# Kernel tuning notes

Hardware: AMD Instinct MI355X
Metric: run time of the kernel (lower is better)

## Reference

```python
import jax, jax.numpy as jnp
import numpy as np

WINDOW = 5  # must be odd so conv 'same' output length == tlength


def setup_inputs() -> dict:
    key = jax.random.key(0)
    tlength = 16777216
    return {"factor": jax.random.normal(key, (tlength,), dtype=jnp.float32)}


def reference(factor):
    window = WINDOW
    # moving average: conv1d with ones kernel, padding=window//2 (== 'same' for odd window)
    w = jnp.ones((window,), dtype=factor.dtype)
    moving_average = jnp.convolve(factor, w, mode='same') / window
    # rate of change: 0 followed by squared consecutive differences
    diffs = (moving_average[:-1] - moving_average[1:]) ** 2
    change = jnp.concatenate([jnp.zeros((1,), dtype=factor.dtype), diffs])
    change = change / jnp.sum(change)
    # power-weighted elementwise scaling
    return (1.0 - change) ** 5 * factor
```

## Files before the change

### kernel.cpp

```cpp
#include <hip/hip_runtime.h>


#define BLOCK 256
#define RGRID 2048
#define NBUCKET 16
#define BUCKET_STRIDE 64

typedef __attribute__((ext_vector_type(4))) float vfloat4;

__device__ __forceinline__ float change_term(const float* __restrict__ f, long long i, long long n) {
    if (i < 1) return 0.0f;
    float a = (i >= 3)    ? f[i - 3] : 0.0f;
    float b = (i + 2 < n) ? f[i + 2] : 0.0f;
    float d = a - b;
    return d * d;
}

__device__ __forceinline__ float pow5(float t) {
    float t2 = t * t;
    float t4 = t2 * t2;
    return t4 * t;
}

__device__ __forceinline__ float vec_terms(float4 p, float4 c, float4 q) {
    float d0 = p.y - c.z;
    float d1 = p.z - c.w;
    float d2 = p.w - q.x;
    float d3 = c.x - q.y;
    return d0 * d0 + d1 * d1 + d2 * d2 + d3 * d3;
}

__device__ __forceinline__ vfloat4 vec_out(float4 p, float4 c, float4 q, float inv) {
    float d0 = p.y - c.z;
    float d1 = p.z - c.w;
    float d2 = p.w - q.x;
    float d3 = c.x - q.y;
    vfloat4 o;
    o.x = pow5(1.0f - d0 * d0 * inv) * c.x;
    o.y = pow5(1.0f - d1 * d1 * inv) * c.y;
    o.z = pow5(1.0f - d2 * d2 * inv) * c.z;
    o.w = pow5(1.0f - d3 * d3 * inv) * c.w;
    return o;
}

__global__ __launch_bounds__(BLOCK)
void reduce_change_kernel(const float* __restrict__ f, int nvec, long long n,
                          float* __restrict__ sum_out) {
    const float4* __restrict__ fv = (const float4*)f;
    const int T = RGRID * BLOCK;
    const int tid = blockIdx.x * BLOCK + threadIdx.x;
    const int M = nvec - 2;
    float acc = 0.0f;

    int idx = tid;
    for (; idx + 3 * T < M; idx += 4 * T) {
        float4 p[4], c[4], q[4];
        #pragma unroll
        for (int u = 0; u < 4; ++u) {
            int v = 1 + idx + u * T;
            p[u] = fv[v - 1];
            c[u] = fv[v];
            q[u] = fv[v + 1];
        }
        #pragma unroll
        for (int u = 0; u < 4; ++u)
            acc += vec_terms(p[u], c[u], q[u]);
    }
    for (; idx < M; idx += T) {
        int v = 1 + idx;
        acc += vec_terms(fv[v - 1], fv[v], fv[v + 1]);
    }
    if (tid == 0) {
        #pragma unroll
        for (int k = 0; k < 4; ++k) acc += change_term(f, k, n);
        long long j0 = n - 4;
        #pragma unroll
        for (int k = 0; k < 4; ++k) acc += change_term(f, j0 + k, n);
    }

    #pragma unroll
    for (int off = 32; off > 0; off >>= 1)
        acc += __shfl_down(acc, off, 64);
    __shared__ float smem[4];
    int lane = threadIdx.x & 63;
    int wave = threadIdx.x >> 6;
    if (lane == 0) smem[wave] = acc;
    __syncthreads();
    if (threadIdx.x == 0) {
        float s = smem[0] + smem[1] + smem[2] + smem[3];
        atomicAdd(&sum_out[(blockIdx.x & (NBUCKET - 1)) * BUCKET_STRIDE], s);
    }
}

__device__ __forceinline__ float bucket_sum(const float* __restrict__ sum_in) {
    float s = 0.0f;
    #pragma unroll
    for (int b = 0; b < NBUCKET; ++b) s += sum_in[b * BUCKET_STRIDE];
    return s;
}

__global__ __launch_bounds__(BLOCK)
void finalize_kernel(const float* __restrict__ f, int nvec, long long n,
                     const float* __restrict__ sum_in,
                     float* __restrict__ out) {
    const float4* __restrict__ fv = (const float4*)f;
    vfloat4* __restrict__ ov = (vfloat4*)out;
    const int M = nvec - 2;
    const int T = (M + 1) >> 1;
    int tid = blockIdx.x * BLOCK + threadIdx.x;
    if (tid < T) {
        int v1 = 1 + tid;
        bool has2 = (tid + T) < M;
        int v2 = has2 ? (1 + tid + T) : v1;
        float4 p1 = fv[v1 - 1], c1 = fv[v1], q1 = fv[v1 + 1];
        float4 p2 = fv[v2 - 1], c2 = fv[v2], q2 = fv[v2 + 1];
        float inv = 1.0f / bucket_sum(sum_in);
        __builtin_nontemporal_store(vec_out(p1, c1, q1, inv), &ov[v1]);
        if (has2) __builtin_nontemporal_store(vec_out(p2, c2, q2, inv), &ov[v2]);
    }
    if (tid == 0) {
        float inv = 1.0f / bucket_sum(sum_in);
        #pragma unroll
        for (int k = 0; k < 4; ++k) {
            float cge = change_term(f, k, n) * inv;
            out[k] = pow5(1.0f - cge) * f[k];
        }
        long long j0 = n - 4;
        #pragma unroll
        for (int k = 0; k < 4; ++k) {
            long long j = j0 + k;
            float cge = change_term(f, j, n) * inv;
            out[j] = pow5(1.0f - cge) * f[j];
        }
    }
}

extern "C" void kernel_launch(void* const* d_in, const int* in_sizes, int n_in,
                              void* d_out, int out_size, void* d_ws, size_t ws_size,
                              hipStream_t stream) {
    const float* f = (const float*)d_in[0];
    float* out = (float*)d_out;
    float* sum_ws = (float*)d_ws;
    long long n = (long long)in_sizes[0];
    int nvec = (int)(n / 4);

    (void)hipMemsetAsync(d_ws, 0, NBUCKET * BUCKET_STRIDE * sizeof(float), stream);

    reduce_change_kernel<<<RGRID, BLOCK, 0, stream>>>(f, nvec, n, sum_ws);

    int M = nvec - 2;
    int T = (M + 1) >> 1;
    int fgrid = (T + BLOCK - 1) / BLOCK;
    finalize_kernel<<<fgrid, BLOCK, 0, stream>>>(f, nvec, n, sum_ws, out);
}
```

Before: 119.2 us.

## Replace atomic buckets with per-block partials and block-level reduction in finalize

The memset and the bucketed atomicAdds are removed. Each reduce block now writes its own partial sum, and every finalize block re-reduces all the partials cooperatively before computing the inverse sum. The finalize kernel now handles four float4 vectors per thread instead of two, and it issues those loads before the partial reduction so memory latency overlaps the sum. This drops one launch (the memset) and the atomic contention, at the cost of each finalize block reading about 8KB of partials and adding two barriers.

```diff
diff --git a/kernel.cpp b/kernel.cpp
--- a/kernel.cpp
+++ b/kernel.cpp
@@ -2,9 +2,7 @@
 
 
 #define BLOCK 256
-#define RGRID 2048
-#define NBUCKET 16
-#define BUCKET_STRIDE 64
+#define RGRID_MAX 2048
 
 typedef __attribute__((ext_vector_type(4))) float vfloat4;
 
@@ -45,9 +43,9 @@
 
 __global__ __launch_bounds__(BLOCK)
 void reduce_change_kernel(const float* __restrict__ f, int nvec, long long n,
-                          float* __restrict__ sum_out) {
+                          float* __restrict__ partials) {
     const float4* __restrict__ fv = (const float4*)f;
-    const int T = RGRID * BLOCK;
+    const int T = gridDim.x * BLOCK;
     const int tid = blockIdx.x * BLOCK + threadIdx.x;
     const int M = nvec - 2;
     float acc = 0.0f;
@@ -86,40 +84,57 @@
     int wave = threadIdx.x >> 6;
     if (lane == 0) smem[wave] = acc;
     __syncthreads();
-    if (threadIdx.x == 0) {
-        float s = smem[0] + smem[1] + smem[2] + smem[3];
-        atomicAdd(&sum_out[(blockIdx.x & (NBUCKET - 1)) * BUCKET_STRIDE], s);
-    }
-}
-
-__device__ __forceinline__ float bucket_sum(const float* __restrict__ sum_in) {
-    float s = 0.0f;
-    #pragma unroll
-    for (int b = 0; b < NBUCKET; ++b) s += sum_in[b * BUCKET_STRIDE];
-    return s;
+    if (threadIdx.x == 0)
+        partials[blockIdx.x] = smem[0] + smem[1] + smem[2] + smem[3];
 }
 
 __global__ __launch_bounds__(BLOCK)
 void finalize_kernel(const float* __restrict__ f, int nvec, long long n,
-                     const float* __restrict__ sum_in,
+                     const float* __restrict__ partials, int npart,
                      float* __restrict__ out) {
     const float4* __restrict__ fv = (const float4*)f;
     vfloat4* __restrict__ ov = (vfloat4*)out;
     const int M = nvec - 2;
-    const int T = (M + 1) >> 1;
-    int tid = blockIdx.x * BLOCK + threadIdx.x;
-    if (tid < T) {
-        int v1 = 1 + tid;
-        bool has2 = (tid + T) < M;
-        int v2 = has2 ? (1 + tid + T) : v1;
-        float4 p1 = fv[v1 - 1], c1 = fv[v1], q1 = fv[v1 + 1];
-        float4 p2 = fv[v2 - 1], c2 = fv[v2], q2 = fv[v2 + 1];
-        float inv = 1.0f / bucket_sum(sum_in);
-        __builtin_nontemporal_store(vec_out(p1, c1, q1, inv), &ov[v1]);
-        if (has2) __builtin_nontemporal_store(vec_out(p2, c2, q2, inv), &ov[v2]);
+    const int T = (M + 3) >> 2;
+    const int tid = blockIdx.x * BLOCK + threadIdx.x;
+
+    bool active = tid < T;
+    int i0 = active ? tid : 0;
+    bool ok1 = active && (i0 + 1 * T < M);
+    bool ok2 = active && (i0 + 2 * T < M);
+    bool ok3 = active && (i0 + 3 * T < M);
+    int v0 = 1 + i0;
+    int v1 = ok1 ? v0 + T : v0;
+    int v2 = ok2 ? v1 + T : v1;
+    int v3 = ok3 ? v2 + T : v2;
+    float4 p0 = fv[v0 - 1], c0 = fv[v0], q0 = fv[v0 + 1];
+    float4 p1 = fv[v1 - 1], c1 = fv[v1], q1 = fv[v1 + 1];
+    float4 p2 = fv[v2 - 1], c2 = fv[v2], q2 = fv[v2 + 1];
+    float4 p3 = fv[v3 - 1], c3 = fv[v3], q3 = fv[v3 + 1];
+
+    float s = 0.0f;
+    for (int k = threadIdx.x; k < npart; k += BLOCK)
+        s += partials[k];
+    #pragma unroll
+    for (int off = 32; off > 0; off >>= 1)
+        s += __shfl_down(s, off, 64);
+    __shared__ float smem[4];
+    __shared__ float stot;
+    int lane = threadIdx.x & 63;
+    int wave = threadIdx.x >> 6;
+    if (lane == 0) smem[wave] = s;
+    __syncthreads();
+    if (threadIdx.x == 0) stot = smem[0] + smem[1] + smem[2] + smem[3];
+    __syncthreads();
+    float inv = 1.0f / stot;
+
+    if (active) {
+        __builtin_nontemporal_store(vec_out(p0, c0, q0, inv), &ov[v0]);
+        if (ok1) __builtin_nontemporal_store(vec_out(p1, c1, q1, inv), &ov[v1]);
+        if (ok2) __builtin_nontemporal_store(vec_out(p2, c2, q2, inv), &ov[v2]);
+        if (ok3) __builtin_nontemporal_store(vec_out(p3, c3, q3, inv), &ov[v3]);
     }
     if (tid == 0) {
-        float inv = 1.0f / bucket_sum(sum_in);
         #pragma unroll
         for (int k = 0; k < 4; ++k) {
             float cge = change_term(f, k, n) * inv;
@@ -140,16 +155,21 @@
                               hipStream_t stream) {
     const float* f = (const float*)d_in[0];
     float* out = (float*)d_out;
-    float* sum_ws = (float*)d_ws;
+    float* partials = (float*)d_ws;
     long long n = (long long)in_sizes[0];
     int nvec = (int)(n / 4);
 
-    (void)hipMemsetAsync(d_ws, 0, NBUCKET * BUCKET_STRIDE * sizeof(float), stream);
+    int rgrid = RGRID_MAX;
+    if (ws_size > 0 && (size_t)rgrid * sizeof(float) > ws_size) {
+        rgrid = (int)(ws_size / sizeof(float));
+        if (rgrid > RGRID_MAX) rgrid = RGRID_MAX;
+        if (rgrid < 1) rgrid = 1;
+    }
 
-    reduce_change_kernel<<<RGRID, BLOCK, 0, stream>>>(f, nvec, n, sum_ws);
+    reduce_change_kernel<<<rgrid, BLOCK, 0, stream>>>(f, nvec, n, partials);
 
     int M = nvec - 2;
-    int T = (M + 1) >> 1;
+    int T = (M + 3) >> 2;
     int fgrid = (T + BLOCK - 1) / BLOCK;
-    finalize_kernel<<<fgrid, BLOCK, 0, stream>>>(f, nvec, n, sum_ws, out);
+    finalize_kernel<<<fgrid, BLOCK, 0, stream>>>(f, nvec, n, partials, rgrid, out);
 }
```

Measured after the change: 123.7 us (median of 2 runs). 1.04x slower.

## Fuse reduction and output pass into one persistent kernel with grid barrier

Applied to the files above, without the earlier changes.

Replaces the memset, the reduction kernel and the finalize kernel with a single persistent kernel sized to occupancy. Each block publishes its partial sum and spins on a global arrival counter, then every block sums all the partials and writes outputs for the same strided elements it read. This removes two launches and the memset, and the input may be re-read partly from cache. The cost is a software grid barrier that depends on all blocks being co-resident, backed by a timeout fallback in which each block redundantly reduces the whole input.

```diff
diff --git a/kernel.cpp b/kernel.cpp
--- a/kernel.cpp
+++ b/kernel.cpp
@@ -2,11 +2,12 @@
 
 
 #define BLOCK 256
-#define RGRID 2048
-#define NBUCKET 16
-#define BUCKET_STRIDE 64
+#define GRID_CAP 2048
 
 typedef __attribute__((ext_vector_type(4))) float vfloat4;
+
+__device__ unsigned int g_arrive = 0u;
+__device__ float g_partials[GRID_CAP];
 
 __device__ __forceinline__ float change_term(const float* __restrict__ f, long long i, long long n) {
     if (i < 1) return 0.0f;
@@ -44,14 +45,16 @@
 }
 
 __global__ __launch_bounds__(BLOCK)
-void reduce_change_kernel(const float* __restrict__ f, int nvec, long long n,
-                          float* __restrict__ sum_out) {
+void fused_onepass(const float* __restrict__ f, int nvec, long long n,
+                   float* __restrict__ out) {
     const float4* __restrict__ fv = (const float4*)f;
-    const int T = RGRID * BLOCK;
+    vfloat4* __restrict__ ov = (vfloat4*)out;
+    const int grid = (int)gridDim.x;
+    const int T = grid * BLOCK;
     const int tid = blockIdx.x * BLOCK + threadIdx.x;
     const int M = nvec - 2;
+
     float acc = 0.0f;
-
     int idx = tid;
     for (; idx + 3 * T < M; idx += 4 * T) {
         float4 p[4], c[4], q[4];
@@ -82,44 +85,76 @@
     for (int off = 32; off > 0; off >>= 1)
         acc += __shfl_down(acc, off, 64);
     __shared__ float smem[4];
-    int lane = threadIdx.x & 63;
-    int wave = threadIdx.x >> 6;
+    __shared__ float s_stot;
+    __shared__ int s_timeout;
+    const int lane = threadIdx.x & 63;
+    const int wave = threadIdx.x >> 6;
     if (lane == 0) smem[wave] = acc;
     __syncthreads();
+
     if (threadIdx.x == 0) {
-        float s = smem[0] + smem[1] + smem[2] + smem[3];
-        atomicAdd(&sum_out[(blockIdx.x & (NBUCKET - 1)) * BUCKET_STRIDE], s);
-    }
-}
-
-__device__ __forceinline__ float bucket_sum(const float* __restrict__ sum_in) {
+        float bp = smem[0] + smem[1] + smem[2] + smem[3];
+        __hip_atomic_store(&g_partials[blockIdx.x], bp,
+                           __ATOMIC_RELAXED, __HIP_MEMORY_SCOPE_AGENT);
+        unsigned int old = __hip_atomic_fetch_add(&g_arrive, 1u,
+                           __ATOMIC_RELEASE, __HIP_MEMORY_SCOPE_AGENT);
+        unsigned int target = (old / (unsigned)grid + 1u) * (unsigned)grid;
+        int timeout = 0;
+        long long polls = 0;
+        while (__hip_atomic_load(&g_arrive, __ATOMIC_ACQUIRE,
+                                 __HIP_MEMORY_SCOPE_AGENT) < target) {
+            __builtin_amdgcn_s_sleep(2);
+            if (++polls > (4LL << 20)) { timeout = 1; break; }
+        }
+        s_timeout = timeout;
+    }
+    __syncthreads();
+
     float s = 0.0f;
+    if (!s_timeout) {
+        for (int k = threadIdx.x; k < grid; k += BLOCK)
+            s += __hip_atomic_load(&g_partials[k], __ATOMIC_RELAXED,
+                                   __HIP_MEMORY_SCOPE_AGENT);
+    } else {
+        for (int v = 1 + (int)threadIdx.x; v < 1 + M; v += BLOCK)
+            s += vec_terms(fv[v - 1], fv[v], fv[v + 1]);
+        if (threadIdx.x == 0) {
+            #pragma unroll
+            for (int k = 0; k < 4; ++k) s += change_term(f, k, n);
+            long long j0 = n - 4;
+            #pragma unroll
+            for (int k = 0; k < 4; ++k) s += change_term(f, j0 + k, n);
+        }
+    }
     #pragma unroll
-    for (int b = 0; b < NBUCKET; ++b) s += sum_in[b * BUCKET_STRIDE];
-    return s;
-}
-
-__global__ __launch_bounds__(BLOCK)
-void finalize_kernel(const float* __restrict__ f, int nvec, long long n,
-                     const float* __restrict__ sum_in,
-                     float* __restrict__ out) {
-    const float4* __restrict__ fv = (const float4*)f;
-    vfloat4* __restrict__ ov = (vfloat4*)out;
-    const int M = nvec - 2;
-    const int T = (M + 1) >> 1;
-    int tid = blockIdx.x * BLOCK + threadIdx.x;
-    if (tid < T) {
-        int v1 = 1 + tid;
-        bool has2 = (tid + T) < M;
-        int v2 = has2 ? (1 + tid + T) : v1;
-        float4 p1 = fv[v1 - 1], c1 = fv[v1], q1 = fv[v1 + 1];
-        float4 p2 = fv[v2 - 1], c2 = fv[v2], q2 = fv[v2 + 1];
-        float inv = 1.0f / bucket_sum(sum_in);
-        __builtin_nontemporal_store(vec_out(p1, c1, q1, inv), &ov[v1]);
-        if (has2) __builtin_nontemporal_store(vec_out(p2, c2, q2, inv), &ov[v2]);
+    for (int off = 32; off > 0; off >>= 1)
+        s += __shfl_down(s, off, 64);
+    if (lane == 0) smem[wave] = s;
+    __syncthreads();
+    if (threadIdx.x == 0) s_stot = smem[0] + smem[1] + smem[2] + smem[3];
+    __syncthreads();
+    const float inv = 1.0f / s_stot;
+
+    idx = tid;
+    for (; idx + 3 * T < M; idx += 4 * T) {
+        float4 p[4], c[4], q[4];
+        #pragma unroll
+        for (int u = 0; u < 4; ++u) {
+            int v = 1 + idx + u * T;
+            p[u] = fv[v - 1];
+            c[u] = fv[v];
+            q[u] = fv[v + 1];
+        }
+        #pragma unroll
+        for (int u = 0; u < 4; ++u)
+            __builtin_nontemporal_store(vec_out(p[u], c[u], q[u], inv),
+                                        &ov[1 + idx + u * T]);
+    }
+    for (; idx < M; idx += T) {
+        int v = 1 + idx;
+        __builtin_nontemporal_store(vec_out(fv[v - 1], fv[v], fv[v + 1], inv), &ov[v]);
     }
     if (tid == 0) {
-        float inv = 1.0f / bucket_sum(sum_in);
         #pragma unroll
         for (int k = 0; k < 4; ++k) {
             float cge = change_term(f, k, n) * inv;
@@ -140,16 +175,26 @@
                               hipStream_t stream) {
     const float* f = (const float*)d_in[0];
     float* out = (float*)d_out;
-    float* sum_ws = (float*)d_ws;
     long long n = (long long)in_sizes[0];
     int nvec = (int)(n / 4);
-
-    (void)hipMemsetAsync(d_ws, 0, NBUCKET * BUCKET_STRIDE * sizeof(float), stream);
-
-    reduce_change_kernel<<<RGRID, BLOCK, 0, stream>>>(f, nvec, n, sum_ws);
-
-    int M = nvec - 2;
-    int T = (M + 1) >> 1;
-    int fgrid = (T + BLOCK - 1) / BLOCK;
-    finalize_kernel<<<fgrid, BLOCK, 0, stream>>>(f, nvec, n, sum_ws, out);
-}
+    (void)d_ws; (void)ws_size;
+
+    static int grid = -1;
+    if (grid < 0) {
+        int dev = 0;
+        (void)hipGetDevice(&dev);
+        int ncu = 0;
+        if (hipDeviceGetAttribute(&ncu, hipDeviceAttributeMultiprocessorCount, dev) != hipSuccess || ncu <= 0)
+            ncu = 256;
+        int bpc = 0;
+        if (hipOccupancyMaxActiveBlocksPerMultiprocessor(&bpc, (const void*)fused_onepass, BLOCK, 0) != hipSuccess
+            || bpc <= 0)
+            bpc = 2;
+        long long g = (long long)bpc * ncu;
+        if (g > GRID_CAP) g = GRID_CAP;
+        if (g < 1) g = 1;
+        grid = (int)g;
+    }
+
+    fused_onepass<<<grid, BLOCK, 0, stream>>>(f, nvec, n, out);
+}
```

Measured after the change: 233.4 us. +95.8%, slower.
